# Optimization experiments

Measured on AMD Instinct MI355X. Metric: run time of the kernel, lower is better.

## Reference

```python
import jax, jax.numpy as jnp
import numpy as np

EMBED = 1024
HEADS = 16
HEAD_DIM = EMBED // HEADS


def setup_inputs() -> dict:
    key = jax.random.key(0)
    ks = jax.random.split(key, 8)
    b, t, d = 2, 2048, EMBED
    s = 1.0 / np.sqrt(d)
    return {
        'k': jax.random.normal(ks[0], (b, t, d), jnp.float32),
        'q': jax.random.normal(ks[1], (b, t, d), jnp.float32),
        'v': jax.random.normal(ks[2], (b, t, d), jnp.float32),
        'Wk': jax.random.normal(ks[3], (d, d), jnp.float32) * s,
        'Wq': jax.random.normal(ks[4], (d, d), jnp.float32) * s,
        'Wv': jax.random.normal(ks[5], (d, d), jnp.float32) * s,
        'Wo': jax.random.normal(ks[6], (d, d), jnp.float32) * s,
        'bo': jax.random.normal(ks[7], (d,), jnp.float32) * 0.01,
    }


def reference(k, q, v, Wk, Wq, Wv, Wo, bo):
    b, t, d = q.shape
    h, n = HEADS, HEAD_DIM
    # projections (q_prj bias=False, k/v bias=False per add_bias_kv=False)
    keys = (k @ Wk.T).reshape(b, t, h, n).transpose(0, 2, 1, 3)      # b h t n
    queries = (q @ Wq.T).reshape(b, t, h, n).transpose(0, 2, 1, 3)
    values = (v @ Wv.T).reshape(b, t, h, n).transpose(0, 2, 1, 3)
    att = jnp.einsum('bhtn,bhsn->bhts', queries, keys)               # b h t t
    att = jax.nn.softmax(att / np.sqrt(n), axis=-1)
    out = jnp.einsum('bhts,bhsn->bhtn', att, values)                 # b h t n
    out = out.transpose(0, 2, 1, 3).reshape(b, t, d)                 # b t (h n)
    return out @ Wo.T + bo
```

## Files before the change

### kernel.cpp

```cpp
#include <hip/hip_runtime.h>
#include <hip/hip_bf16.h>


typedef unsigned short u16;
typedef unsigned int   u32;
using short8 = __attribute__((ext_vector_type(8))) short;
using f32x4  = __attribute__((ext_vector_type(4))) float;

__device__ __forceinline__ u16 f2b(float f) {
    u32 u = __float_as_uint(f);
    u += 0x7FFFu + ((u >> 16) & 1u);
    return (u16)(u >> 16);
}
__device__ __forceinline__ u32 pack2(float lo, float hi) {
    union { __hip_bfloat162 h; u32 u; } c;
    c.h = __float22bfloat162_rn(make_float2(lo, hi));
    return c.u;
}
__device__ __forceinline__ uint4 stage8(const float* p) {
    float4 a = *(const float4*)p;
    float4 b = *(const float4*)(p + 4);
    uint4 v;
    v.x = pack2(a.x, a.y); v.y = pack2(a.z, a.w);
    v.z = pack2(b.x, b.y); v.w = pack2(b.z, b.w);
    return v;
}
__device__ __forceinline__ uint4 stage8(const u16* p) { return *(const uint4*)p; }

__device__ __forceinline__ void gld_lds16(const u16* g, u16* l) {
    __builtin_amdgcn_global_load_lds(
        (const __attribute__((address_space(1))) void*)g,
        (__attribute__((address_space(3))) void*)l, 16, 0, 0);
}

__global__ __launch_bounds__(256) void convert_kernel(
    const float* s0, const float* s1, const float* s2, const float* s3,
    const float* s4, const float* s5, const float* s6,
    u16* d0, u16* d1, u16* d2, u16* d3, u16* d4, u16* d5, u16* d6)
{
    const int y = blockIdx.y;
    const float* s; u16* d; u32 n;
    switch (y) {
        case 0: s = s0; d = d0; n = 1048576; break;
        case 1: s = s1; d = d1; n = 1048576; break;
        case 2: s = s2; d = d2; n = 1048576; break;
        case 3: s = s3; d = d3; n = 262144; break;
        case 4: s = s4; d = d4; n = 262144; break;
        case 5: s = s5; d = d5; n = 262144; break;
        default: s = s6; d = d6; n = 262144; break;
    }
    for (u32 i = blockIdx.x * 256 + threadIdx.x; i < n; i += 256 * 1024) {
        float4 f = ((const float4*)s)[i];
        uint2 o; o.x = pack2(f.x, f.y); o.y = pack2(f.z, f.w);
        ((uint2*)d)[i] = o;
    }
}

template <int MODE>
__device__ __forceinline__ void gemm_epilogue(
    f32x4 (&acc)[4][4], void* __restrict__ C, const float* __restrict__ bias,
    float scale, u32 bm, u32 bn, int wr, int wc, int ml, int g)
{
    constexpr u32 N = 1024;
    if (MODE == 1) {
        const u32 bb = bm >> 11;
#pragma unroll
        for (int ct = 0; ct < 4; ++ct) {
            const u32 col = bn + wc * 64 + ct * 16 + ml;
            const u32 cb = ((bb * 16 + (col >> 6)) * 64 + (col & 63)) * 2048;
#pragma unroll
            for (int it = 0; it < 4; ++it) {
                const u32 trow = (bm & 2047) + wr * 64 + it * 16 + g * 4;
                ((u32*)C)[(cb + trow) >> 1]     = pack2(acc[it][ct][0], acc[it][ct][1]);
                ((u32*)C)[(cb + trow + 2) >> 1] = pack2(acc[it][ct][2], acc[it][ct][3]);
            }
        }
    } else {
#pragma unroll
        for (int ct = 0; ct < 4; ++ct) {
            const u32 col = bn + wc * 64 + ct * 16 + ml;
            const float bv = bias ? bias[col] : 0.0f;
#pragma unroll
            for (int it = 0; it < 4; ++it) {
                const u32 row = bm + wr * 64 + it * 16 + g * 4;
#pragma unroll
                for (int r = 0; r < 4; ++r) {
                    const float v = acc[it][ct][r] * scale + bv;
                    if (MODE == 2) ((float*)C)[(size_t)(row + r) * N + col] = v;
                    else           ((u16*)C)[(size_t)(row + r) * N + col] = f2b(v);
                }
            }
        }
    }
}

template <int MODE>
__device__ __forceinline__ void gemm_fast(
    const u16* __restrict__ A, const u16* __restrict__ W,
    void* __restrict__ C, const float* __restrict__ bias, float scale)
{
    constexpr u32 K = 1024;
    __shared__ u16 As[128 * 32];
    __shared__ u16 Bs[128 * 32];

    const int tid  = threadIdx.x;
    const int lane = tid & 63;
    const int w    = tid >> 6;
    const int wr   = w >> 1, wc = w & 1;
    const int ml   = lane & 15, g = lane >> 4;
    const u32 bm   = blockIdx.y * 128, bn = blockIdx.x * 128;

    f32x4 acc[4][4] = {};

    const u32 arow = w * 32 + (lane >> 2);
    const u32 acol = (lane & 3) * 8;
    const u16* gA = A + (size_t)(bm + arow) * K + acol;
    const u16* gB = W + (size_t)(bn + arow) * K + acol;
    u16* lA = &As[w * 1024];
    u16* lB = &Bs[w * 1024];

    for (u32 k0 = 0; k0 < K; k0 += 32) {
        __syncthreads();
        gld_lds16(gA + k0, lA);
        gld_lds16(gA + 16 * K + k0, lA + 512);
        gld_lds16(gB + k0, lB);
        gld_lds16(gB + 16 * K + k0, lB + 512);
        __syncthreads();

        short8 af[4], bf[4];
#pragma unroll
        for (int it = 0; it < 4; ++it)
            af[it] = *(const short8*)&As[(wr * 64 + it * 16 + ml) * 32 + g * 8];
#pragma unroll
        for (int ct = 0; ct < 4; ++ct)
            bf[ct] = *(const short8*)&Bs[(wc * 64 + ct * 16 + ml) * 32 + g * 8];
#pragma unroll
        for (int it = 0; it < 4; ++it)
#pragma unroll
            for (int ct = 0; ct < 4; ++ct)
                acc[it][ct] = __builtin_amdgcn_mfma_f32_16x16x32_bf16(
                    af[it], bf[ct], acc[it][ct], 0, 0, 0);
    }
    gemm_epilogue<MODE>(acc, C, bias, scale, bm, bn, wr, wc, ml, g);
}

__global__ __launch_bounds__(256) void proj3_fast_kernel(
    const u16* kb, const u16* qb, const u16* vb,
    const u16* Wkb, const u16* Wqb, const u16* Wvb,
    u16* Kp, u16* Qp, u16* Vt)
{
    if (blockIdx.z == 0)      gemm_fast<0>(kb, Wkb, Kp, nullptr, 1.0f);
    else if (blockIdx.z == 1) gemm_fast<0>(qb, Wqb, Qp, nullptr, 0.18033688011112042f);
    else                      gemm_fast<1>(vb, Wvb, Vt, nullptr, 1.0f);
}

__global__ __launch_bounds__(256) void out_fast_kernel(
    const u16* A, const u16* W, float* C, const float* bias)
{
    gemm_fast<2>(A, W, C, bias, 1.0f);
}

#define LDT 40
template <typename TA, int MODE>
__device__ __forceinline__ void gemm_conv(
    const TA* __restrict__ A, const float* __restrict__ W,
    void* __restrict__ C, const float* __restrict__ bias, float scale)
{
    constexpr u32 K = 1024;
    __shared__ u16 As[128 * LDT];
    __shared__ u16 Bs[128 * LDT];

    const int tid  = threadIdx.x;
    const int lane = tid & 63;
    const int w    = tid >> 6;
    const int wr   = w >> 1, wc = w & 1;
    const int ml   = lane & 15, g = lane >> 4;
    const u32 bm   = blockIdx.y * 128, bn = blockIdx.x * 128;

    f32x4 acc[4][4] = {};
    const int r0 = tid >> 2;
    const int kc = tid & 3;
    const TA*    gA = A + (size_t)(bm + r0) * K + kc * 8;
    const float* gB = W + (size_t)(bn + r0) * K + kc * 8;

    for (u32 k0 = 0; k0 < K; k0 += 32) {
        __syncthreads();
        *(uint4*)&As[r0 * LDT + kc * 8]        = stage8(gA + k0);
        *(uint4*)&As[(r0 + 64) * LDT + kc * 8] = stage8(gA + (size_t)64 * K + k0);
        *(uint4*)&Bs[r0 * LDT + kc * 8]        = stage8(gB + k0);
        *(uint4*)&Bs[(r0 + 64) * LDT + kc * 8] = stage8(gB + (size_t)64 * K + k0);
        __syncthreads();

        short8 af[4], bf[4];
#pragma unroll
        for (int it = 0; it < 4; ++it)
            af[it] = *(const short8*)&As[(wr * 64 + it * 16 + ml) * LDT + g * 8];
#pragma unroll
        for (int ct = 0; ct < 4; ++ct)
            bf[ct] = *(const short8*)&Bs[(wc * 64 + ct * 16 + ml) * LDT + g * 8];
#pragma unroll
        for (int it = 0; it < 4; ++it)
#pragma unroll
            for (int ct = 0; ct < 4; ++ct)
                acc[it][ct] = __builtin_amdgcn_mfma_f32_16x16x32_bf16(
                    af[it], bf[ct], acc[it][ct], 0, 0, 0);
    }
    gemm_epilogue<MODE>(acc, C, bias, scale, bm, bn, wr, wc, ml, g);
}

__global__ __launch_bounds__(256) void proj3_conv_kernel(
    const float* kin, const float* qin, const float* vin,
    const float* Wk, const float* Wq, const float* Wv,
    u16* Kp, u16* Qp, u16* Vt)
{
    if (blockIdx.z == 0)      gemm_conv<float, 0>(kin, Wk, Kp, nullptr, 1.0f);
    else if (blockIdx.z == 1) gemm_conv<float, 0>(qin, Wq, Qp, nullptr, 0.18033688011112042f);
    else                      gemm_conv<float, 1>(vin, Wv, Vt, nullptr, 1.0f);
}

__global__ __launch_bounds__(256) void out_conv_kernel(
    const u16* A, const float* W, float* C, const float* bias)
{
    gemm_conv<u16, 2>(A, W, C, bias, 1.0f);
}

#define STR 72

__global__ __launch_bounds__(256) void attn_kernel(
    const u16* __restrict__ Qp, const u16* __restrict__ Kp,
    const u16* __restrict__ Vt, u16* __restrict__ Op)
{
    constexpr u32 T = 2048, D = 1024;
    __shared__ u16 Qs[64 * STR];
    __shared__ u16 Ks[64 * STR];
    __shared__ u16 Vts[64 * STR];
    __shared__ u16 Ps[4 * 16 * STR];

    const int tid  = threadIdx.x;
    const int lane = tid & 63;
    const int w    = tid >> 6;
    const int ml   = lane & 15;
    const int g    = lane >> 4;
    const u32 bh   = blockIdx.y;
    const u32 b    = bh >> 4, h = bh & 15;
    const u32 t0   = blockIdx.x * 64;

    const u32 base  = b * T * D + h * 64;
    const u32 vbase = bh * 64 * 2048;

    const u32 a0 = tid >> 3, cc = tid & 7;
    {
        const u32 go = base + (t0 + a0) * D + cc * 8;
        *(uint4*)&Qs[a0 * STR + cc * 8]        = *(const uint4*)&Qp[go];
        *(uint4*)&Qs[(a0 + 32) * STR + cc * 8] = *(const uint4*)&Qp[go + 32 * D];
    }
    __syncthreads();

    short8 bq0 = *(const short8*)&Qs[(w * 16 + ml) * STR + g * 8];
    short8 bq1 = *(const short8*)&Qs[(w * 16 + ml) * STR + 32 + g * 8];

    f32x4 oacc[4] = {};
    float l_i = 0.0f;
    u16* Pw = &Ps[w * 16 * STR];
    u32* Pw32 = (u32*)Pw;

    u32 kOff = base + a0 * D + cc * 8;
    u32 vOff = vbase + a0 * 2048 + cc * 8;

    for (int st = 0; st < 32; ++st) {
        __syncthreads();
        *(uint4*)&Ks[a0 * STR + cc * 8]         = *(const uint4*)&Kp[kOff];
        *(uint4*)&Ks[(a0 + 32) * STR + cc * 8]  = *(const uint4*)&Kp[kOff + 32 * D];
        *(uint4*)&Vts[a0 * STR + cc * 8]        = *(const uint4*)&Vt[vOff];
        *(uint4*)&Vts[(a0 + 32) * STR + cc * 8] = *(const uint4*)&Vt[vOff + 32 * 2048];
        kOff += 64 * D;
        vOff += 64;
        __syncthreads();

        f32x4 sacc[4];
#pragma unroll
        for (int i = 0; i < 4; ++i) {
            short8 ka0 = *(const short8*)&Ks[(i * 16 + ml) * STR + g * 8];
            short8 ka1 = *(const short8*)&Ks[(i * 16 + ml) * STR + 32 + g * 8];
            f32x4 z = {};
            z = __builtin_amdgcn_mfma_f32_16x16x32_bf16(ka0, bq0, z, 0, 0, 0);
            sacc[i] = __builtin_amdgcn_mfma_f32_16x16x32_bf16(ka1, bq1, z, 0, 0, 0);
        }

        float s0 = 0.0f;
#pragma unroll
        for (int i = 0; i < 4; ++i)
#pragma unroll
            for (int r = 0; r < 4; ++r) {
                const float p = exp2f(sacc[i][r]);
                sacc[i][r] = p;
                s0 += p;
            }
        s0 += __shfl_xor(s0, 16);
        s0 += __shfl_xor(s0, 32);
        l_i += s0;

#pragma unroll
        for (int i = 0; i < 4; ++i) {
            Pw32[ml * (STR / 2) + i * 8 + g * 2 + 0] = pack2(sacc[i][0], sacc[i][1]);
            Pw32[ml * (STR / 2) + i * 8 + g * 2 + 1] = pack2(sacc[i][2], sacc[i][3]);
        }
        short8 bp0 = *(const short8*)&Pw[ml * STR + g * 8];
        short8 bp1 = *(const short8*)&Pw[ml * STR + 32 + g * 8];

#pragma unroll
        for (int dt = 0; dt < 4; ++dt) {
            short8 va0 = *(const short8*)&Vts[(dt * 16 + ml) * STR + g * 8];
            short8 va1 = *(const short8*)&Vts[(dt * 16 + ml) * STR + 32 + g * 8];
            oacc[dt] = __builtin_amdgcn_mfma_f32_16x16x32_bf16(va0, bp0, oacc[dt], 0, 0, 0);
            oacc[dt] = __builtin_amdgcn_mfma_f32_16x16x32_bf16(va1, bp1, oacc[dt], 0, 0, 0);
        }
    }

    const float inv = 1.0f / l_i;
    const u32 row = (b * T + t0 + w * 16 + ml) * D + h * 64;
#pragma unroll
    for (int dt = 0; dt < 4; ++dt) {
        const u32 cidx = row + dt * 16 + g * 4;
        *(u32*)&Op[cidx]     = pack2(oacc[dt][0] * inv, oacc[dt][1] * inv);
        *(u32*)&Op[cidx + 2] = pack2(oacc[dt][2] * inv, oacc[dt][3] * inv);
    }
}

extern "C" void kernel_launch(void* const* d_in, const int* in_sizes, int n_in,
                              void* d_out, int out_size, void* d_ws, size_t ws_size,
                              hipStream_t stream)
{
    const float* kin = (const float*)d_in[0];
    const float* qin = (const float*)d_in[1];
    const float* vin = (const float*)d_in[2];
    const float* Wk  = (const float*)d_in[3];
    const float* Wq  = (const float*)d_in[4];
    const float* Wv  = (const float*)d_in[5];
    const float* Wo  = (const float*)d_in[6];
    const float* bo  = (const float*)d_in[7];
    float* out = (float*)d_out;

    const size_t ACT = 4194304;
    const size_t WSZ = 1048576;

    if (ws_size >= (3 * ACT + 4 * WSZ + 3 * ACT) * sizeof(u16)) {
        u16* kb  = (u16*)d_ws;
        u16* qb  = kb + ACT;
        u16* vb  = qb + ACT;
        u16* Wkb = vb + ACT;
        u16* Wqb = Wkb + WSZ;
        u16* Wvb = Wqb + WSZ;
        u16* Wob = Wvb + WSZ;
        u16* Kp  = Wob + WSZ;
        u16* Qp  = Kp + ACT;
        u16* Vt  = Qp + ACT;
        u16* Op  = kb;

        convert_kernel<<<dim3(1024, 7), 256, 0, stream>>>(
            kin, qin, vin, Wk, Wq, Wv, Wo, kb, qb, vb, Wkb, Wqb, Wvb, Wob);
        proj3_fast_kernel<<<dim3(8, 32, 3), 256, 0, stream>>>(
            kb, qb, vb, Wkb, Wqb, Wvb, Kp, Qp, Vt);
        attn_kernel<<<dim3(32, 32), 256, 0, stream>>>(Qp, Kp, Vt, Op);
        out_fast_kernel<<<dim3(8, 32), 256, 0, stream>>>(Op, Wob, out, bo);
    } else {
        u16* Kp = (u16*)d_ws;
        u16* Qp = Kp + ACT;
        u16* Vt = Qp + ACT;
        u16* Op = Vt + ACT;
        proj3_conv_kernel<<<dim3(8, 32, 3), 256, 0, stream>>>(
            kin, qin, vin, Wk, Wq, Wv, Kp, Qp, Vt);
        attn_kernel<<<dim3(32, 32), 256, 0, stream>>>(Qp, Kp, Vt, Op);
        out_conv_kernel<<<dim3(8, 32), 256, 0, stream>>>(Op, Wo, out, bo);
    }
}
```

Measured before the change: 259.5 us.

## Fuse activation conversion into projection GEMM and restructure attention to key-split waves

Removes the separate fp32-to-bf16 conversion of k/q/v activations. The projection GEMM now loads fp32 directly and packs to bf16 into padded LDS, while only the weights are still pre-converted. The attention kernel now processes 128-key tiles, with each wave owning a key slice for all 64 queries. Partial outputs and row sums are then reduced across waves through shared memory, with a swizzled P staging layout. This trades an extra memory pass for register-path conversion in the GEMM and a final cross-wave reduction with additional syncs and register pressure.

After: 284.4 us. 1.1x slower.

```diff
diff --git a/kernel.cpp b/kernel.cpp
--- a/kernel.cpp
+++ b/kernel.cpp
@@ -25,35 +25,27 @@
     v.z = pack2(b.x, b.y); v.w = pack2(b.z, b.w);
     return v;
 }
-__device__ __forceinline__ uint4 stage8(const u16* p) { return *(const uint4*)p; }
-
 __device__ __forceinline__ void gld_lds16(const u16* g, u16* l) {
     __builtin_amdgcn_global_load_lds(
         (const __attribute__((address_space(1))) void*)g,
         (__attribute__((address_space(3))) void*)l, 16, 0, 0);
 }
 
-__global__ __launch_bounds__(256) void convert_kernel(
+__global__ __launch_bounds__(256) void convert_w_kernel(
     const float* s0, const float* s1, const float* s2, const float* s3,
-    const float* s4, const float* s5, const float* s6,
-    u16* d0, u16* d1, u16* d2, u16* d3, u16* d4, u16* d5, u16* d6)
-{
-    const int y = blockIdx.y;
-    const float* s; u16* d; u32 n;
-    switch (y) {
-        case 0: s = s0; d = d0; n = 1048576; break;
-        case 1: s = s1; d = d1; n = 1048576; break;
-        case 2: s = s2; d = d2; n = 1048576; break;
-        case 3: s = s3; d = d3; n = 262144; break;
-        case 4: s = s4; d = d4; n = 262144; break;
-        case 5: s = s5; d = d5; n = 262144; break;
-        default: s = s6; d = d6; n = 262144; break;
-    }
-    for (u32 i = blockIdx.x * 256 + threadIdx.x; i < n; i += 256 * 1024) {
-        float4 f = ((const float4*)s)[i];
-        uint2 o; o.x = pack2(f.x, f.y); o.y = pack2(f.z, f.w);
-        ((uint2*)d)[i] = o;
-    }
+    u16* d0, u16* d1, u16* d2, u16* d3)
+{
+    const float* s; u16* d;
+    switch (blockIdx.y) {
+        case 0: s = s0; d = d0; break;
+        case 1: s = s1; d = d1; break;
+        case 2: s = s2; d = d2; break;
+        default: s = s3; d = d3; break;
+    }
+    const u32 i = blockIdx.x * 256 + threadIdx.x;
+    float4 f = ((const float4*)s)[i];
+    uint2 o; o.x = pack2(f.x, f.y); o.y = pack2(f.z, f.w);
+    ((uint2*)d)[i] = o;
 }
 
 template <int MODE>
@@ -95,12 +87,12 @@
 }
 
 template <int MODE>
-__device__ __forceinline__ void gemm_fast(
-    const u16* __restrict__ A, const u16* __restrict__ W,
-    void* __restrict__ C, const float* __restrict__ bias, float scale)
+__device__ __forceinline__ void gemm_proj(
+    const float* __restrict__ A, const u16* __restrict__ W,
+    void* __restrict__ C, float scale)
 {
     constexpr u32 K = 1024;
-    __shared__ u16 As[128 * 32];
+    __shared__ u16 As[128 * 40];
     __shared__ u16 Bs[128 * 32];
 
     const int tid  = threadIdx.x;
@@ -112,17 +104,17 @@
 
     f32x4 acc[4][4] = {};
 
-    const u32 arow = w * 32 + (lane >> 2);
-    const u32 acol = (lane & 3) * 8;
-    const u16* gA = A + (size_t)(bm + arow) * K + acol;
-    const u16* gB = W + (size_t)(bn + arow) * K + acol;
-    u16* lA = &As[w * 1024];
+    const u32 r0 = tid >> 1, hh = tid & 1;
+    const float* gA = A + (size_t)(bm + r0) * K + hh * 16;
+    u16* lA = &As[r0 * 40 + hh * 16];
+
+    const u16* gB = W + (size_t)(bn + w * 32 + (lane >> 2)) * K + (lane & 3) * 8;
     u16* lB = &Bs[w * 1024];
 
     for (u32 k0 = 0; k0 < K; k0 += 32) {
         __syncthreads();
-        gld_lds16(gA + k0, lA);
-        gld_lds16(gA + 16 * K + k0, lA + 512);
+        *(uint4*)lA       = stage8(gA + k0);
+        *(uint4*)(lA + 8) = stage8(gA + k0 + 8);
         gld_lds16(gB + k0, lB);
         gld_lds16(gB + 16 * K + k0, lB + 512);
         __syncthreads();
@@ -130,7 +122,7 @@
         short8 af[4], bf[4];
 #pragma unroll
         for (int it = 0; it < 4; ++it)
-            af[it] = *(const short8*)&As[(wr * 64 + it * 16 + ml) * 32 + g * 8];
+            af[it] = *(const short8*)&As[(wr * 64 + it * 16 + ml) * 40 + g * 8];
 #pragma unroll
         for (int ct = 0; ct < 4; ++ct)
             bf[ct] = *(const short8*)&Bs[(wc * 64 + ct * 16 + ml) * 32 + g * 8];
@@ -141,34 +133,26 @@
                 acc[it][ct] = __builtin_amdgcn_mfma_f32_16x16x32_bf16(
                     af[it], bf[ct], acc[it][ct], 0, 0, 0);
     }
-    gemm_epilogue<MODE>(acc, C, bias, scale, bm, bn, wr, wc, ml, g);
-}
-
-__global__ __launch_bounds__(256) void proj3_fast_kernel(
-    const u16* kb, const u16* qb, const u16* vb,
+    gemm_epilogue<MODE>(acc, C, nullptr, scale, bm, bn, wr, wc, ml, g);
+}
+
+__global__ __launch_bounds__(256) void proj3_kernel(
+    const float* kin, const float* qin, const float* vin,
     const u16* Wkb, const u16* Wqb, const u16* Wvb,
     u16* Kp, u16* Qp, u16* Vt)
 {
-    if (blockIdx.z == 0)      gemm_fast<0>(kb, Wkb, Kp, nullptr, 1.0f);
-    else if (blockIdx.z == 1) gemm_fast<0>(qb, Wqb, Qp, nullptr, 0.18033688011112042f);
-    else                      gemm_fast<1>(vb, Wvb, Vt, nullptr, 1.0f);
-}
-
-__global__ __launch_bounds__(256) void out_fast_kernel(
-    const u16* A, const u16* W, float* C, const float* bias)
-{
-    gemm_fast<2>(A, W, C, bias, 1.0f);
-}
-
-#define LDT 40
-template <typename TA, int MODE>
-__device__ __forceinline__ void gemm_conv(
-    const TA* __restrict__ A, const float* __restrict__ W,
-    void* __restrict__ C, const float* __restrict__ bias, float scale)
+    if (blockIdx.z == 0)      gemm_proj<0>(kin, Wkb, Kp, 1.0f);
+    else if (blockIdx.z == 1) gemm_proj<0>(qin, Wqb, Qp, 0.18033688011112042f);
+    else                      gemm_proj<1>(vin, Wvb, Vt, 1.0f);
+}
+
+__global__ __launch_bounds__(256) void out_gemm_kernel(
+    const u16* __restrict__ A, const u16* __restrict__ W,
+    float* __restrict__ C, const float* __restrict__ bias)
 {
     constexpr u32 K = 1024;
-    __shared__ u16 As[128 * LDT];
-    __shared__ u16 Bs[128 * LDT];
+    __shared__ u16 As[128 * 32];
+    __shared__ u16 Bs[128 * 32];
 
     const int tid  = threadIdx.x;
     const int lane = tid & 63;
@@ -178,26 +162,28 @@
     const u32 bm   = blockIdx.y * 128, bn = blockIdx.x * 128;
 
     f32x4 acc[4][4] = {};
-    const int r0 = tid >> 2;
-    const int kc = tid & 3;
-    const TA*    gA = A + (size_t)(bm + r0) * K + kc * 8;
-    const float* gB = W + (size_t)(bn + r0) * K + kc * 8;
+
+    const u32 srow = w * 32 + (lane >> 2), scol = (lane & 3) * 8;
+    const u16* gA = A + (size_t)(bm + srow) * K + scol;
+    const u16* gB = W + (size_t)(bn + srow) * K + scol;
+    u16* lA = &As[w * 1024];
+    u16* lB = &Bs[w * 1024];
 
     for (u32 k0 = 0; k0 < K; k0 += 32) {
         __syncthreads();
-        *(uint4*)&As[r0 * LDT + kc * 8]        = stage8(gA + k0);
-        *(uint4*)&As[(r0 + 64) * LDT + kc * 8] = stage8(gA + (size_t)64 * K + k0);
-        *(uint4*)&Bs[r0 * LDT + kc * 8]        = stage8(gB + k0);
-        *(uint4*)&Bs[(r0 + 64) * LDT + kc * 8] = stage8(gB + (size_t)64 * K + k0);
+        gld_lds16(gA + k0, lA);
+        gld_lds16(gA + 16 * K + k0, lA + 512);
+        gld_lds16(gB + k0, lB);
+        gld_lds16(gB + 16 * K + k0, lB + 512);
         __syncthreads();
 
         short8 af[4], bf[4];
 #pragma unroll
         for (int it = 0; it < 4; ++it)
-            af[it] = *(const short8*)&As[(wr * 64 + it * 16 + ml) * LDT + g * 8];
+            af[it] = *(const short8*)&As[(wr * 64 + it * 16 + ml) * 32 + g * 8];
 #pragma unroll
         for (int ct = 0; ct < 4; ++ct)
-            bf[ct] = *(const short8*)&Bs[(wc * 64 + ct * 16 + ml) * LDT + g * 8];
+            bf[ct] = *(const short8*)&Bs[(wc * 64 + ct * 16 + ml) * 32 + g * 8];
 #pragma unroll
         for (int it = 0; it < 4; ++it)
 #pragma unroll
@@ -205,36 +191,18 @@
                 acc[it][ct] = __builtin_amdgcn_mfma_f32_16x16x32_bf16(
                     af[it], bf[ct], acc[it][ct], 0, 0, 0);
     }
-    gemm_epilogue<MODE>(acc, C, bias, scale, bm, bn, wr, wc, ml, g);
-}
-
-__global__ __launch_bounds__(256) void proj3_conv_kernel(
-    const float* kin, const float* qin, const float* vin,
-    const float* Wk, const float* Wq, const float* Wv,
-    u16* Kp, u16* Qp, u16* Vt)
-{
-    if (blockIdx.z == 0)      gemm_conv<float, 0>(kin, Wk, Kp, nullptr, 1.0f);
-    else if (blockIdx.z == 1) gemm_conv<float, 0>(qin, Wq, Qp, nullptr, 0.18033688011112042f);
-    else                      gemm_conv<float, 1>(vin, Wv, Vt, nullptr, 1.0f);
-}
-
-__global__ __launch_bounds__(256) void out_conv_kernel(
-    const u16* A, const float* W, float* C, const float* bias)
-{
-    gemm_conv<u16, 2>(A, W, C, bias, 1.0f);
-}
-
-#define STR 72
+    gemm_epilogue<2>(acc, C, bias, 1.0f, bm, bn, wr, wc, ml, g);
+}
 
 __global__ __launch_bounds__(256) void attn_kernel(
     const u16* __restrict__ Qp, const u16* __restrict__ Kp,
     const u16* __restrict__ Vt, u16* __restrict__ Op)
 {
     constexpr u32 T = 2048, D = 1024;
-    __shared__ u16 Qs[64 * STR];
-    __shared__ u16 Ks[64 * STR];
-    __shared__ u16 Vts[64 * STR];
-    __shared__ u16 Ps[4 * 16 * STR];
+    __shared__ u16 pool[26112];
+    u16* Ks  = pool;
+    u16* Vts = pool + 9216;
+    u16* QP  = pool + 17920;
 
     const int tid  = threadIdx.x;
     const int lane = tid & 63;
@@ -248,83 +216,134 @@
     const u32 base  = b * T * D + h * 64;
     const u32 vbase = bh * 64 * 2048;
 
-    const u32 a0 = tid >> 3, cc = tid & 7;
     {
-        const u32 go = base + (t0 + a0) * D + cc * 8;
-        *(uint4*)&Qs[a0 * STR + cc * 8]        = *(const uint4*)&Qp[go];
-        *(uint4*)&Qs[(a0 + 32) * STR + cc * 8] = *(const uint4*)&Qp[go + 32 * D];
-    }
-    __syncthreads();
-
-    short8 bq0 = *(const short8*)&Qs[(w * 16 + ml) * STR + g * 8];
-    short8 bq1 = *(const short8*)&Qs[(w * 16 + ml) * STR + 32 + g * 8];
-
-    f32x4 oacc[4] = {};
-    float l_i = 0.0f;
-    u16* Pw = &Ps[w * 16 * STR];
-    u32* Pw32 = (u32*)Pw;
-
-    u32 kOff = base + a0 * D + cc * 8;
-    u32 vOff = vbase + a0 * 2048 + cc * 8;
-
-    for (int st = 0; st < 32; ++st) {
-        __syncthreads();
-        *(uint4*)&Ks[a0 * STR + cc * 8]         = *(const uint4*)&Kp[kOff];
-        *(uint4*)&Ks[(a0 + 32) * STR + cc * 8]  = *(const uint4*)&Kp[kOff + 32 * D];
-        *(uint4*)&Vts[a0 * STR + cc * 8]        = *(const uint4*)&Vt[vOff];
-        *(uint4*)&Vts[(a0 + 32) * STR + cc * 8] = *(const uint4*)&Vt[vOff + 32 * 2048];
-        kOff += 64 * D;
-        vOff += 64;
-        __syncthreads();
-
-        f32x4 sacc[4];
-#pragma unroll
-        for (int i = 0; i < 4; ++i) {
-            short8 ka0 = *(const short8*)&Ks[(i * 16 + ml) * STR + g * 8];
-            short8 ka1 = *(const short8*)&Ks[(i * 16 + ml) * STR + 32 + g * 8];
-            f32x4 z = {};
-            z = __builtin_amdgcn_mfma_f32_16x16x32_bf16(ka0, bq0, z, 0, 0, 0);
-            sacc[i] = __builtin_amdgcn_mfma_f32_16x16x32_bf16(ka1, bq1, z, 0, 0, 0);
-        }
-
-        float s0 = 0.0f;
-#pragma unroll
-        for (int i = 0; i < 4; ++i)
-#pragma unroll
-            for (int r = 0; r < 4; ++r) {
-                const float p = exp2f(sacc[i][r]);
-                sacc[i][r] = p;
-                s0 += p;
+        const u32 qr = tid >> 3, cc = tid & 7;
+        const u32 go = base + (t0 + qr) * D + cc * 8;
+        *(uint4*)&QP[qr * 72 + cc * 8]        = *(const uint4*)&Qp[go];
+        *(uint4*)&QP[(qr + 32) * 72 + cc * 8] = *(const uint4*)&Qp[go + 32 * D];
+    }
+    __syncthreads();
+    short8 bq[4][2];
+#pragma unroll
+    for (int qt = 0; qt < 4; ++qt) {
+        bq[qt][0] = *(const short8*)&QP[(qt * 16 + ml) * 72 + g * 8];
+        bq[qt][1] = *(const short8*)&QP[(qt * 16 + ml) * 72 + 32 + g * 8];
+    }
+
+    f32x4 oacc[4][4] = {};
+    float l4[4] = {};
+
+    u16* Pst = &QP[w * 2048];
+    u32* Pst32 = (u32*)Pst;
+    const int swz_w = (ml >> 1) & 3;
+
+    const u32 kr = tid >> 3, kcc = tid & 7;
+    const u32 vd = tid >> 2, vsc = tid & 3;
+
+    u32 kOff = base + kr * D + kcc * 8;
+    u32 vOff = vbase + vd * 2048 + vsc * 32;
+
+    for (int it = 0; it < 16; ++it) {
+        __syncthreads();
+#pragma unroll
+        for (int j = 0; j < 4; ++j)
+            *(uint4*)&Ks[(kr + j * 32) * 72 + kcc * 8] =
+                *(const uint4*)&Kp[kOff + j * 32 * D];
+#pragma unroll
+        for (int j = 0; j < 4; ++j)
+            *(uint4*)&Vts[vd * 136 + vsc * 32 + j * 8] =
+                *(const uint4*)&Vt[vOff + j * 8];
+        kOff += 128 * D;
+        vOff += 128;
+        __syncthreads();
+
+#pragma unroll
+        for (int hf = 0; hf < 2; ++hf) {
+            short8 ka0 = *(const short8*)&Ks[(hf * 64 + w * 16 + ml) * 72 + g * 8];
+            short8 ka1 = *(const short8*)&Ks[(hf * 64 + w * 16 + ml) * 72 + 32 + g * 8];
+            const int Qd0 = hf * 2 + (g >> 1);
+            const u32 pbase = ml * 16 + (u32)(((Qd0 ^ swz_w) << 2) | ((g & 1) << 1));
+#pragma unroll
+            for (int qt = 0; qt < 4; ++qt) {
+                f32x4 z = {};
+                z = __builtin_amdgcn_mfma_f32_16x16x32_bf16(ka0, bq[qt][0], z, 0, 0, 0);
+                z = __builtin_amdgcn_mfma_f32_16x16x32_bf16(ka1, bq[qt][1], z, 0, 0, 0);
+                float p0 = exp2f(z[0]), p1 = exp2f(z[1]);
+                float p2 = exp2f(z[2]), p3 = exp2f(z[3]);
+                l4[qt] += (p0 + p1) + (p2 + p3);
+                Pst32[qt * 256 + pbase]     = pack2(p0, p1);
+                Pst32[qt * 256 + pbase + 1] = pack2(p2, p3);
             }
-        s0 += __shfl_xor(s0, 16);
-        s0 += __shfl_xor(s0, 32);
-        l_i += s0;
-
-#pragma unroll
-        for (int i = 0; i < 4; ++i) {
-            Pw32[ml * (STR / 2) + i * 8 + g * 2 + 0] = pack2(sacc[i][0], sacc[i][1]);
-            Pw32[ml * (STR / 2) + i * 8 + g * 2 + 1] = pack2(sacc[i][2], sacc[i][3]);
-        }
-        short8 bp0 = *(const short8*)&Pw[ml * STR + g * 8];
-        short8 bp1 = *(const short8*)&Pw[ml * STR + 32 + g * 8];
-
+        }
+
+        short8 pb[4];
+#pragma unroll
+        for (int qt = 0; qt < 4; ++qt) {
+            const u32 q = qt * 16 + ml;
+            pb[qt] = *(const short8*)&Pst[q * 32 + ((g ^ ((q >> 1) & 3)) * 8)];
+        }
 #pragma unroll
         for (int dt = 0; dt < 4; ++dt) {
-            short8 va0 = *(const short8*)&Vts[(dt * 16 + ml) * STR + g * 8];
-            short8 va1 = *(const short8*)&Vts[(dt * 16 + ml) * STR + 32 + g * 8];
-            oacc[dt] = __builtin_amdgcn_mfma_f32_16x16x32_bf16(va0, bp0, oacc[dt], 0, 0, 0);
-            oacc[dt] = __builtin_amdgcn_mfma_f32_16x16x32_bf16(va1, bp1, oacc[dt], 0, 0, 0);
-        }
-    }
-
-    const float inv = 1.0f / l_i;
-    const u32 row = (b * T + t0 + w * 16 + ml) * D + h * 64;
-#pragma unroll
-    for (int dt = 0; dt < 4; ++dt) {
-        const u32 cidx = row + dt * 16 + g * 4;
-        *(u32*)&Op[cidx]     = pack2(oacc[dt][0] * inv, oacc[dt][1] * inv);
-        *(u32*)&Op[cidx + 2] = pack2(oacc[dt][2] * inv, oacc[dt][3] * inv);
-    }
+            short8 va = *(const short8*)&Vts[(dt * 16 + ml) * 136 +
+                                             (g >> 1) * 64 + w * 16 + (g & 1) * 8];
+#pragma unroll
+            for (int qt = 0; qt < 4; ++qt)
+                oacc[dt][qt] = __builtin_amdgcn_mfma_f32_16x16x32_bf16(
+                    va, pb[qt], oacc[dt][qt], 0, 0, 0);
+        }
+    }
+
+    __syncthreads();
+    float* R0 = (float*)pool;
+    float* R1 = R0 + 4096;
+    float* Lr = R1 + 4096;
+
+#pragma unroll
+    for (int qt = 0; qt < 4; ++qt) {
+        l4[qt] += __shfl_xor(l4[qt], 16);
+        l4[qt] += __shfl_xor(l4[qt], 32);
+    }
+    if (g == 0) {
+#pragma unroll
+        for (int qt = 0; qt < 4; ++qt) Lr[w * 64 + qt * 16 + ml] = l4[qt];
+    }
+
+#define WRITE_R(Rp)                                                          \
+    {_Pragma("unroll") for (int dt = 0; dt < 4; ++dt)                        \
+     _Pragma("unroll") for (int qt = 0; qt < 4; ++qt)                        \
+     _Pragma("unroll") for (int r = 0; r < 4; ++r)                           \
+        (Rp)[(dt * 16 + g * 4 + r) * 64 + qt * 16 + ml] = oacc[dt][qt][r];}
+#define ADD_R(Rp)                                                            \
+    {_Pragma("unroll") for (int dt = 0; dt < 4; ++dt)                        \
+     _Pragma("unroll") for (int qt = 0; qt < 4; ++qt)                        \
+     _Pragma("unroll") for (int r = 0; r < 4; ++r)                           \
+        oacc[dt][qt][r] += (Rp)[(dt * 16 + g * 4 + r) * 64 + qt * 16 + ml];}
+
+    if (w == 1) WRITE_R(R0)
+    if (w == 3) WRITE_R(R1)
+    __syncthreads();
+    if (w == 0) ADD_R(R0)
+    if (w == 2) ADD_R(R1)
+    __syncthreads();
+    if (w == 2) WRITE_R(R0)
+    __syncthreads();
+    if (w == 0) {
+        ADD_R(R0)
+#pragma unroll
+        for (int qt = 0; qt < 4; ++qt) {
+            const u32 q = qt * 16 + ml;
+            const float inv = 1.0f / (Lr[q] + Lr[64 + q] + Lr[128 + q] + Lr[192 + q]);
+            const u32 row = (b * T + t0 + q) * D + h * 64;
+#pragma unroll
+            for (int dt = 0; dt < 4; ++dt) {
+                const u32 ci = row + dt * 16 + g * 4;
+                *(u32*)&Op[ci]     = pack2(oacc[dt][qt][0] * inv, oacc[dt][qt][1] * inv);
+                *(u32*)&Op[ci + 2] = pack2(oacc[dt][qt][2] * inv, oacc[dt][qt][3] * inv);
+            }
+        }
+    }
+#undef WRITE_R
+#undef ADD_R
 }
 
 extern "C" void kernel_launch(void* const* d_in, const int* in_sizes, int n_in,
@@ -341,36 +360,18 @@
     const float* bo  = (const float*)d_in[7];
     float* out = (float*)d_out;
 
-    const size_t ACT = 4194304;
-    const size_t WSZ = 1048576;
-
-    if (ws_size >= (3 * ACT + 4 * WSZ + 3 * ACT) * sizeof(u16)) {
-        u16* kb  = (u16*)d_ws;
-        u16* qb  = kb + ACT;
-        u16* vb  = qb + ACT;
-        u16* Wkb = vb + ACT;
-        u16* Wqb = Wkb + WSZ;
-        u16* Wvb = Wqb + WSZ;
-        u16* Wob = Wvb + WSZ;
-        u16* Kp  = Wob + WSZ;
-        u16* Qp  = Kp + ACT;
-        u16* Vt  = Qp + ACT;
-        u16* Op  = kb;
-
-        convert_kernel<<<dim3(1024, 7), 256, 0, stream>>>(
-            kin, qin, vin, Wk, Wq, Wv, Wo, kb, qb, vb, Wkb, Wqb, Wvb, Wob);
-        proj3_fast_kernel<<<dim3(8, 32, 3), 256, 0, stream>>>(
-            kb, qb, vb, Wkb, Wqb, Wvb, Kp, Qp, Vt);
-        attn_kernel<<<dim3(32, 32), 256, 0, stream>>>(Qp, Kp, Vt, Op);
-        out_fast_kernel<<<dim3(8, 32), 256, 0, stream>>>(Op, Wob, out, bo);
-    } else {
-        u16* Kp = (u16*)d_ws;
-        u16* Qp = Kp + ACT;
-        u16* Vt = Qp + ACT;
-        u16* Op = Vt + ACT;
-        proj3_conv_kernel<<<dim3(8, 32, 3), 256, 0, stream>>>(
-            kin, qin, vin, Wk, Wq, Wv, Kp, Qp, Vt);
-        attn_kernel<<<dim3(32, 32), 256, 0, stream>>>(Qp, Kp, Vt, Op);
-        out_conv_kernel<<<dim3(8, 32), 256, 0, stream>>>(Op, Wo, out, bo);
-    }
-}
+    u16* Wkb = (u16*)d_ws;
+    u16* Wqb = Wkb + 1048576;
+    u16* Wvb = Wqb + 1048576;
+    u16* Wob = Wvb + 1048576;
+    u16* Kp  = Wob + 1048576;
+    u16* Qp  = Kp + 4194304;
+    u16* Vt  = Qp + 4194304;
+
+    convert_w_kernel<<<dim3(1024, 4), 256, 0, stream>>>(
+        Wk, Wq, Wv, Wo, Wkb, Wqb, Wvb, Wob);
+    proj3_kernel<<<dim3(8, 32, 3), 256, 0, stream>>>(
+        kin, qin, vin, Wkb, Wqb, Wvb, Kp, Qp, Vt);
+    attn_kernel<<<dim3(32, 32), 256, 0, stream>>>(Qp, Kp, Vt, Qp);
+    out_gemm_kernel<<<dim3(8, 32), 256, 0, stream>>>(Qp, Wob, out, bo);
+}
```
